# Kernel tuning notes

Hardware: AMD Instinct MI355X
Metric: run time of the kernel (lower is better)

The kernel has to match this reference:

```python
import jax, jax.numpy as jnp
import numpy as np

N_UNITS = 524288
BATCH = 16384


def setup_inputs() -> dict:
    key = jax.random.key(0)
    ks = jax.random.split(key, 10)
    left_feats = jax.random.normal(ks[0], (N_UNITS, 9), dtype=jnp.float32)
    right_feats = jax.random.normal(ks[1], (N_UNITS, 9), dtype=jnp.float32)
    left_seg = jnp.sort(jax.random.randint(ks[2], (N_UNITS,), 0, BATCH, dtype=jnp.int32))
    right_seg = jnp.sort(jax.random.randint(ks[3], (N_UNITS,), 0, BATCH, dtype=jnp.int32))
    W1 = jax.random.normal(ks[4], (9, 64), dtype=jnp.float32) * (1.0 / np.sqrt(9))
    b1 = jax.random.normal(ks[5], (64,), dtype=jnp.float32) * 0.01
    Wc1 = jax.random.normal(ks[6], (128, 32), dtype=jnp.float32) * (1.0 / np.sqrt(128))
    bc1 = jax.random.normal(ks[7], (32,), dtype=jnp.float32) * 0.01
    Wc2 = jax.random.normal(ks[8], (32, 1), dtype=jnp.float32) * (1.0 / np.sqrt(32))
    bc2 = jax.random.normal(ks[9], (1,), dtype=jnp.float32) * 0.01
    return {"left_feats": left_feats, "right_feats": right_feats,
            "left_seg": left_seg, "right_seg": right_seg,
            "W1": W1, "b1": b1, "Wc1": Wc1, "bc1": bc1, "Wc2": Wc2, "bc2": bc2}


def _pooled_features(feats, seg, W1, b1):
    # per-unit MLP 9 -> 64 with ReLU, then ragged sum-pool per instance
    h = jax.nn.relu(feats @ W1 + b1)                      # [N, 64]
    return jax.ops.segment_sum(h, seg, num_segments=BATCH)  # [B, 64]


def reference(left_feats, right_feats, left_seg, right_seg, W1, b1, Wc1, bc1, Wc2, bc2):
    left = _pooled_features(left_feats, left_seg, W1, b1)    # [B, 64]
    right = _pooled_features(right_feats, right_seg, W1, b1)  # [B, 64]
    combined = jnp.concatenate([left, right], axis=1)         # [B, 128]
    hidden = jax.nn.relu(combined @ Wc1 + bc1)                # [B, 32]
    logits = hidden @ Wc2 + bc2                               # [B, 1]
    return jax.nn.sigmoid(jnp.squeeze(logits, axis=-1))       # [B]
```

## Files before the change

### kernel.cpp

```cpp
#include <hip/hip_runtime.h>
#include <math.h>

#define BATCH_C 16384
#define SPW 2

typedef float f32x4  __attribute__((ext_vector_type(4)));
typedef f32x4 __attribute__((aligned(4))) f32x4_u;
typedef float f32x16 __attribute__((ext_vector_type(16)));
typedef short s16x8  __attribute__((ext_vector_type(8)));

typedef union { unsigned u[4]; s16x8 v; } abfrag_t;

static __device__ inline unsigned rlo_f(float x) {
    unsigned u = __float_as_uint(x);
    return (u + 0x7fffu + ((u >> 16) & 1u)) >> 16;
}
static __device__ inline unsigned rhi_f(float x) {
    unsigned u = __float_as_uint(x);
    return (u + 0x7fffu + ((u >> 16) & 1u)) & 0xffff0000u;
}

__global__ __launch_bounds__(256) void seg_starts_kernel(
    const int* __restrict__ lseg, const int* __restrict__ rseg, int n,
    int* __restrict__ lstart, int* __restrict__ rstart)
{
    const int* __restrict__ seg = blockIdx.y ? rseg : lseg;
    int* __restrict__ start = blockIdx.y ? rstart : lstart;
    int i = blockIdx.x * blockDim.x + threadIdx.x;
    if (i >= n) return;
    int s = seg[i];
    int prev = (i == 0) ? -1 : seg[i - 1];
    for (int b = prev + 1; b <= s; ++b) start[b] = i;
    if (i == n - 1) {
        for (int b = s + 1; b <= BATCH_C; ++b) start[b] = n;
    }
}

__global__ __launch_bounds__(256, 2) void fused_kernel(
    const float* __restrict__ lfeats, const float* __restrict__ rfeats,
    const int* __restrict__ lstart, const int* __restrict__ rstart,
    const float* __restrict__ W1, const float* __restrict__ b1,
    const float* __restrict__ Wc1, const float* __restrict__ bc1,
    const float* __restrict__ Wc2, const float* __restrict__ bc2,
    float* __restrict__ out, int nunits)
{
    const int lane = threadIdx.x & 63;
    const int wv   = threadIdx.x >> 6;
    const int S0   = (blockIdx.x * 4 + wv) * SPW;
    const int r    = lane & 31;
    const int hh   = lane >> 5;
    const int nmax = nunits - 1;
    const int ofs1 = hh ? 5 : 4;

    __shared__ __align__(16) short sBh[2][32][16];
    __shared__ __align__(16) short sBl[2][32][16];
    __shared__ __align__(16) float rowbuf[4][SPW][128];

    {
        const int t    = threadIdx.x;
        const int tile = t >> 7;
        const int col  = (t >> 2) & 31;
        const int k0   = (t & 3) * 4;
        const int ch   = tile * 32 + col;
#pragma unroll
        for (int q = 0; q < 4; ++q) {
            const int k = k0 + q;
            float v = 0.0f;
            if (k < 9) v = W1[k * 64 + ch];
            else if (k == 9) v = b1[ch];
            unsigned hi = rlo_f(v);
            float d = v - __uint_as_float(hi << 16);
            sBh[tile][col][k] = (short)hi;
            sBl[tile][col][k] = (short)rlo_f(d);
        }
    }
    __syncthreads();

    const s16x8 bh0 = *reinterpret_cast<const s16x8*>(&sBh[0][r][hh * 8]);
    const s16x8 bh1 = *reinterpret_cast<const s16x8*>(&sBh[1][r][hh * 8]);
    const s16x8 bl0 = *reinterpret_cast<const s16x8*>(&sBl[0][r][hh * 8]);
    const s16x8 bl1 = *reinterpret_cast<const s16x8*>(&sBl[1][r][hh * 8]);

    const f32x16 kZ = (f32x16)0.0f;

    rowbuf[wv][0][lane] = 0.0f;  rowbuf[wv][0][64 + lane] = 0.0f;
    rowbuf[wv][1][lane] = 0.0f;  rowbuf[wv][1][64 + lane] = 0.0f;

    const int bidx = S0 + (lane <= SPW ? lane : SPW);
    const int svl = lstart[bidx];
    const int svr = rstart[bidx];
    const int sLv = __shfl(svl, 0, 64);
    const int e1L = __shfl(svl, 1, 64);
    const int e2L = __shfl(svl, 2, 64);
    const int sRv = __shfl(svr, 0, 64);
    const int e1R = __shfl(svr, 1, 64);
    const int e2R = __shfl(svr, 2, 64);
    const int endL = e2L, endR = e2R;

#define FETCH_(F, POS, Q0,Q1,Q2,Q3,Q4,Q5,Q6,Q7) do {                      \
        int u_ = (POS) + r; if (u_ > nmax) u_ = nmax;                     \
        const float* fp_ = (F) + (size_t)u_ * 9;                          \
        f32x4 x0_ = *reinterpret_cast<const f32x4_u*>(fp_);               \
        f32x4 x1_ = *reinterpret_cast<const f32x4_u*>(fp_ + ofs1);        \
        Q0 = hh ? x1_.w : x0_.x;                                          \
        Q1 = x0_.y; Q2 = x0_.z; Q3 = x0_.w;                               \
        Q4 = x1_.x; Q5 = x1_.y; Q6 = x1_.z; Q7 = x1_.w;                   \
    } while (0)

#define CONV_(Q0,Q1,Q2,Q3,Q4,Q5,Q6,Q7, CNT, AH, AL) do {                  \
    unsigned u0_=__float_as_uint(Q0), u1_=__float_as_uint(Q1),            \
             u2_=__float_as_uint(Q2), u3_=__float_as_uint(Q3),            \
             u4_=__float_as_uint(Q4), u5_=__float_as_uint(Q5),            \
             u6_=__float_as_uint(Q6), u7_=__float_as_uint(Q7);            \
    float d0_=Q0-__uint_as_float(u0_&0xffff0000u);                        \
    float d1_=Q1-__uint_as_float(u1_&0xffff0000u);                        \
    float d2_=Q2-__uint_as_float(u2_&0xffff0000u);                        \
    float d3_=Q3-__uint_as_float(u3_&0xffff0000u);                        \
    float d4_=Q4-__uint_as_float(u4_&0xffff0000u);                        \
    float d5_=Q5-__uint_as_float(u5_&0xffff0000u);                        \
    float d6_=Q6-__uint_as_float(u6_&0xffff0000u);                        \
    float d7_=Q7-__uint_as_float(u7_&0xffff0000u);                        \
    unsigned h01_=(u0_>>16)|(hh?0x3F800000u:(u1_&0xffff0000u));           \
    unsigned l01_=rlo_f(d0_)|(hh?0u:rhi_f(d1_));                          \
    unsigned h23_=(u2_>>16)|(u3_&0xffff0000u);                            \
    unsigned h45_=(u4_>>16)|(u5_&0xffff0000u);                            \
    unsigned h67_=(u6_>>16)|(u7_&0xffff0000u);                            \
    unsigned l23_=rlo_f(d2_)|rhi_f(d3_);                                  \
    unsigned l45_=rlo_f(d4_)|rhi_f(d5_);                                  \
    unsigned l67_=rlo_f(d6_)|rhi_f(d7_);                                  \
    const bool v_ = (r < (CNT));                                          \
    const bool k_ = v_ && (hh == 0);                                      \
    AH.u[0]=v_?h01_:0u; AL.u[0]=v_?l01_:0u;                               \
    AH.u[1]=k_?h23_:0u; AL.u[1]=k_?l23_:0u;                               \
    AH.u[2]=k_?h45_:0u; AL.u[2]=k_?l45_:0u;                               \
    AH.u[3]=k_?h67_:0u; AL.u[3]=k_?l67_:0u;                               \
} while (0)

#define MFMAEPI_(AH, AL, A0, A1) do {                                     \
    f32x16 c0_ = __builtin_amdgcn_mfma_f32_32x32x16_bf16(AL.v, bh0, kZ, 0,0,0); \
    c0_ = __builtin_amdgcn_mfma_f32_32x32x16_bf16(AH.v, bl0, c0_, 0,0,0); \
    c0_ = __builtin_amdgcn_mfma_f32_32x32x16_bf16(AH.v, bh0, c0_, 0,0,0); \
    f32x16 c1_ = __builtin_amdgcn_mfma_f32_32x32x16_bf16(AL.v, bh1, kZ, 0,0,0); \
    c1_ = __builtin_amdgcn_mfma_f32_32x32x16_bf16(AH.v, bl1, c1_, 0,0,0); \
    c1_ = __builtin_amdgcn_mfma_f32_32x32x16_bf16(AH.v, bh1, c1_, 0,0,0); \
    float sA_=0.f,sB_=0.f,sC_=0.f,sD_=0.f,tA_=0.f,tB_=0.f,tC_=0.f,tD_=0.f;\
    _Pragma("unroll")                                                     \
    for (int t_=0; t_<4; ++t_) {                                          \
        sA_+=fmaxf(c0_[t_],0.f);    sB_+=fmaxf(c0_[t_+4],0.f);            \
        sC_+=fmaxf(c0_[t_+8],0.f);  sD_+=fmaxf(c0_[t_+12],0.f);           \
        tA_+=fmaxf(c1_[t_],0.f);    tB_+=fmaxf(c1_[t_+4],0.f);            \
        tC_+=fmaxf(c1_[t_+8],0.f);  tD_+=fmaxf(c1_[t_+12],0.f);           \
    }                                                                     \
    A0 += (sA_+sB_)+(sC_+sD_);                                            \
    A1 += (tA_+tB_)+(tC_+tD_);                                            \
} while (0)

#define STEP_(S) do {                                                     \
    int cnt_ = ec##S - base##S; if (cnt_ > 32) cnt_ = 32;                 \
    abfrag_t AH_, AL_;                                                    \
    CONV_(p0##S,p1##S,p2##S,p3##S,p4##S,p5##S,p6##S,p7##S, cnt_, AH_, AL_);\
    int nxt_ = base##S + cnt_;                                            \
    int fpos_ = (nxt_ < end##S) ? nxt_ : 0;  \
    FETCH_(f##S, fpos_, p0##S,p1##S,p2##S,p3##S,p4##S,p5##S,p6##S,p7##S); \
    MFMAEPI_(AH_, AL_, ac0##S, ac1##S);                                   \
    base##S = nxt_;                                                       \
} while (0)

#define FLUSH_(S, SIDEOFS) do {                                           \
    if (base##S >= ec##S) {                                               \
        ac0##S += __shfl_xor(ac0##S, 32, 64);                             \
        ac1##S += __shfl_xor(ac1##S, 32, 64);                             \
        if (cs##S < SPW)                                                  \
            rowbuf[wv][cs##S][(SIDEOFS) + lane] = hh ? ac1##S : ac0##S;   \
        ac0##S = 0.0f; ac1##S = 0.0f;                                     \
        ++cs##S; ec##S = e2##S;                                           \
    }                                                                     \
} while (0)

    const float* __restrict__ fL = lfeats;
    const float* __restrict__ fR = rfeats;
    int baseL = sLv, baseR = sRv;
    int csL, ecL, csR, ecR;
    if (baseL >= e1L) { csL = 1; ecL = e2L; } else { csL = 0; ecL = e1L; }
    if (baseR >= e1R) { csR = 1; ecR = e2R; } else { csR = 0; ecR = e1R; }
    float ac0L = 0.f, ac1L = 0.f, ac0R = 0.f, ac1R = 0.f;
    float p0L=0,p1L=0,p2L=0,p3L=0,p4L=0,p5L=0,p6L=0,p7L=0;
    float p0R=0,p1R=0,p2R=0,p3R=0,p4R=0,p5R=0,p6R=0,p7R=0;

    if (baseL < endL) FETCH_(fL, baseL, p0L,p1L,p2L,p3L,p4L,p5L,p6L,p7L);
    if (baseR < endR) FETCH_(fR, baseR, p0R,p1R,p2R,p3R,p4R,p5R,p6R,p7R);

    bool aL = baseL < endL, aR = baseR < endR;
    while (aL && aR) {
        STEP_(L);
        STEP_(R);
        FLUSH_(L, 0);
        FLUSH_(R, 64);
        aL = baseL < endL; aR = baseR < endR;
    }
    while (aL) { STEP_(L); FLUSH_(L, 0);  aL = baseL < endL; }
    while (aR) { STEP_(R); FLUSH_(R, 64); aR = baseR < endR; }

#undef FLUSH_
#undef STEP_
#undef MFMAEPI_
#undef CONV_
#undef FETCH_

    asm volatile("s_waitcnt lgkmcnt(0)" ::: "memory");

    {
        const int j = lane & 31;
        const float* __restrict__ rb = &rowbuf[wv][hh][0];
        const float* __restrict__ wc = Wc1 + j;

        float accA = bc1[j], accB = 0.0f;
#pragma unroll 8
        for (int k = 0; k < 128; k += 4) {
            f32x4 v = *reinterpret_cast<const f32x4*>(rb + k);
            accA = fmaf(v.x, wc[(k + 0) * 32], accA);
            accB = fmaf(v.y, wc[(k + 1) * 32], accB);
            accA = fmaf(v.z, wc[(k + 2) * 32], accA);
            accB = fmaf(v.w, wc[(k + 3) * 32], accB);
        }
        float hsv = fmaxf(accA + accB, 0.0f) * Wc2[j];
#pragma unroll
        for (int off = 16; off > 0; off >>= 1) hsv += __shfl_xor(hsv, off, 64);

        if (j == 0) {
            float logit = hsv + bc2[0];
            out[S0 + hh] = 1.0f / (1.0f + expf(-logit));
        }
    }
}

extern "C" void kernel_launch(void* const* d_in, const int* in_sizes, int n_in,
                              void* d_out, int out_size, void* d_ws, size_t ws_size,
                              hipStream_t stream)
{
    const float* lfeats = (const float*)d_in[0];
    const float* rfeats = (const float*)d_in[1];
    const int*   lseg   = (const int*)d_in[2];
    const int*   rseg   = (const int*)d_in[3];
    const float* W1     = (const float*)d_in[4];
    const float* b1     = (const float*)d_in[5];
    const float* Wc1    = (const float*)d_in[6];
    const float* bc1    = (const float*)d_in[7];
    const float* Wc2    = (const float*)d_in[8];
    const float* bc2    = (const float*)d_in[9];
    float* out = (float*)d_out;

    const int n = in_sizes[2];

    int* lstart = (int*)d_ws;
    int* rstart = lstart + (BATCH_C + 16);

    seg_starts_kernel<<<dim3((n + 255) / 256, 2), 256, 0, stream>>>(
        lseg, rseg, n, lstart, rstart);

    fused_kernel<<<BATCH_C / (SPW * 4), 256, 0, stream>>>(
        lfeats, rfeats, lstart, rstart, W1, b1, Wc1, bc1, Wc2, bc2, out, n);
}
```

Baseline: 37.33 us.

## Partition pooling by fixed unit windows with boundary partials and separate head kernel

```diff
diff --git a/kernel.cpp b/kernel.cpp
--- a/kernel.cpp
+++ b/kernel.cpp
@@ -2,66 +2,53 @@
 #include <math.h>
 
 #define BATCH_C 16384
-#define SPW 2
+#define UPW 128
 
 typedef float f32x4  __attribute__((ext_vector_type(4)));
 typedef f32x4 __attribute__((aligned(4))) f32x4_u;
 typedef float f32x16 __attribute__((ext_vector_type(16)));
 typedef short s16x8  __attribute__((ext_vector_type(8)));
-
 typedef union { unsigned u[4]; s16x8 v; } abfrag_t;
 
 static __device__ inline unsigned rlo_f(float x) {
     unsigned u = __float_as_uint(x);
     return (u + 0x7fffu + ((u >> 16) & 1u)) >> 16;
 }
-static __device__ inline unsigned rhi_f(float x) {
-    unsigned u = __float_as_uint(x);
-    return (u + 0x7fffu + ((u >> 16) & 1u)) & 0xffff0000u;
-}
-
-__global__ __launch_bounds__(256) void seg_starts_kernel(
-    const int* __restrict__ lseg, const int* __restrict__ rseg, int n,
-    int* __restrict__ lstart, int* __restrict__ rstart)
-{
-    const int* __restrict__ seg = blockIdx.y ? rseg : lseg;
-    int* __restrict__ start = blockIdx.y ? rstart : lstart;
-    int i = blockIdx.x * blockDim.x + threadIdx.x;
-    if (i >= n) return;
-    int s = seg[i];
-    int prev = (i == 0) ? -1 : seg[i - 1];
-    for (int b = prev + 1; b <= s; ++b) start[b] = i;
-    if (i == n - 1) {
-        for (int b = s + 1; b <= BATCH_C; ++b) start[b] = n;
-    }
-}
-
-__global__ __launch_bounds__(256, 2) void fused_kernel(
+
+__global__ __launch_bounds__(256, 4) void pool_dense(
     const float* __restrict__ lfeats, const float* __restrict__ rfeats,
-    const int* __restrict__ lstart, const int* __restrict__ rstart,
+    const int* __restrict__ lseg, const int* __restrict__ rseg,
+    int* __restrict__ lstart, int* __restrict__ rstart,
     const float* __restrict__ W1, const float* __restrict__ b1,
-    const float* __restrict__ Wc1, const float* __restrict__ bc1,
-    const float* __restrict__ Wc2, const float* __restrict__ bc2,
-    float* __restrict__ out, int nunits)
+    float* __restrict__ pooled,
+    float* __restrict__ pFl, float* __restrict__ pLl,
+    float* __restrict__ pFr, float* __restrict__ pLr,
+    int n)
 {
     const int lane = threadIdx.x & 63;
     const int wv   = threadIdx.x >> 6;
-    const int S0   = (blockIdx.x * 4 + wv) * SPW;
+    const int side = blockIdx.y;
+    const int wgid = blockIdx.x * 4 + wv;
+    const int lo   = wgid * UPW;
     const int r    = lane & 31;
     const int hh   = lane >> 5;
-    const int nmax = nunits - 1;
+    const int nmax = n - 1;
     const int ofs1 = hh ? 5 : 4;
+    const unsigned khi = hh ? 0u : 0xffffffffu;
+    const int sideofs = side * 64;
+
+    const float* __restrict__ feats = side ? rfeats : lfeats;
+    const int*   __restrict__ sg    = side ? rseg : lseg;
+    int* __restrict__ stw  = side ? rstart : lstart;
+    float* __restrict__ pFs = side ? pFr : pFl;
+    float* __restrict__ pLs = side ? pLr : pLl;
 
     __shared__ __align__(16) short sBh[2][32][16];
     __shared__ __align__(16) short sBl[2][32][16];
-    __shared__ __align__(16) float rowbuf[4][SPW][128];
-
     {
-        const int t    = threadIdx.x;
-        const int tile = t >> 7;
-        const int col  = (t >> 2) & 31;
-        const int k0   = (t & 3) * 4;
-        const int ch   = tile * 32 + col;
+        const int t = threadIdx.x;
+        const int tile = t >> 7, col = (t >> 2) & 31, k0 = (t & 3) * 4;
+        const int ch = tile * 32 + col;
 #pragma unroll
         for (int q = 0; q < 4; ++q) {
             const int k = k0 + q;
@@ -75,31 +62,33 @@
         }
     }
     __syncthreads();
-
     const s16x8 bh0 = *reinterpret_cast<const s16x8*>(&sBh[0][r][hh * 8]);
     const s16x8 bh1 = *reinterpret_cast<const s16x8*>(&sBh[1][r][hh * 8]);
     const s16x8 bl0 = *reinterpret_cast<const s16x8*>(&sBl[0][r][hh * 8]);
     const s16x8 bl1 = *reinterpret_cast<const s16x8*>(&sBl[1][r][hh * 8]);
-
     const f32x16 kZ = (f32x16)0.0f;
 
-    rowbuf[wv][0][lane] = 0.0f;  rowbuf[wv][0][64 + lane] = 0.0f;
-    rowbuf[wv][1][lane] = 0.0f;  rowbuf[wv][1][64 + lane] = 0.0f;
-
-    const int bidx = S0 + (lane <= SPW ? lane : SPW);
-    const int svl = lstart[bidx];
-    const int svr = rstart[bidx];
-    const int sLv = __shfl(svl, 0, 64);
-    const int e1L = __shfl(svl, 1, 64);
-    const int e2L = __shfl(svl, 2, 64);
-    const int sRv = __shfl(svr, 0, 64);
-    const int e1R = __shfl(svr, 1, 64);
-    const int e2R = __shfl(svr, 2, 64);
-    const int endL = e2L, endR = e2R;
-
-#define FETCH_(F, POS, Q0,Q1,Q2,Q3,Q4,Q5,Q6,Q7) do {                      \
-        int u_ = (POS) + r; if (u_ > nmax) u_ = nmax;                     \
-        const float* fp_ = (F) + (size_t)u_ * 9;                          \
+    const int u0 = lo + lane, u1 = lo + 64 + lane;
+    const int s0v = sg[u0 > nmax ? nmax : u0];
+    const int s1v = sg[u1 > nmax ? nmax : u1];
+    const int p0v = sg[u0 > 0 ? u0 - 1 : 0];
+    const int p1v = sg[(u1 - 1) > nmax ? nmax : (u1 - 1)];
+    {
+        int pe0 = (u0 == 0) ? -1 : p0v;
+        for (int b = pe0 + 1; b <= s0v; ++b) stw[b] = u0;
+        for (int b = p1v + 1; b <= s1v; ++b) stw[b] = u1;
+        if (u1 == nmax) for (int b = s1v + 1; b <= BATCH_C; ++b) stw[b] = n;
+    }
+    const bool bd0 = (lane != 0) && (s0v != p0v);
+    const bool bd1 = (s1v != p1v);
+    const unsigned long long mm0 = __ballot(bd0);
+    const unsigned long long mm1 = __ballot(bd1);
+    const unsigned wm0 = (unsigned)mm0, wm1 = (unsigned)(mm0 >> 32);
+    const unsigned wm2 = (unsigned)mm1, wm3 = (unsigned)(mm1 >> 32);
+
+#define FETCHD(POS, Q0,Q1,Q2,Q3,Q4,Q5,Q6,Q7) do {                         \
+        int uu_ = (POS) + r; if (uu_ > nmax) uu_ = nmax;                  \
+        const float* fp_ = feats + (size_t)uu_ * 9;                       \
         f32x4 x0_ = *reinterpret_cast<const f32x4_u*>(fp_);               \
         f32x4 x1_ = *reinterpret_cast<const f32x4_u*>(fp_ + ofs1);        \
         Q0 = hh ? x1_.w : x0_.x;                                          \
@@ -107,7 +96,7 @@
         Q4 = x1_.x; Q5 = x1_.y; Q6 = x1_.z; Q7 = x1_.w;                   \
     } while (0)
 
-#define CONV_(Q0,Q1,Q2,Q3,Q4,Q5,Q6,Q7, CNT, AH, AL) do {                  \
+#define CONVD(Q0,Q1,Q2,Q3,Q4,Q5,Q6,Q7, AH, AL) do {                       \
     unsigned u0_=__float_as_uint(Q0), u1_=__float_as_uint(Q1),            \
              u2_=__float_as_uint(Q2), u3_=__float_as_uint(Q3),            \
              u4_=__float_as_uint(Q4), u5_=__float_as_uint(Q5),            \
@@ -120,29 +109,27 @@
     float d5_=Q5-__uint_as_float(u5_&0xffff0000u);                        \
     float d6_=Q6-__uint_as_float(u6_&0xffff0000u);                        \
     float d7_=Q7-__uint_as_float(u7_&0xffff0000u);                        \
-    unsigned h01_=(u0_>>16)|(hh?0x3F800000u:(u1_&0xffff0000u));           \
-    unsigned l01_=rlo_f(d0_)|(hh?0u:rhi_f(d1_));                          \
-    unsigned h23_=(u2_>>16)|(u3_&0xffff0000u);                            \
-    unsigned h45_=(u4_>>16)|(u5_&0xffff0000u);                            \
-    unsigned h67_=(u6_>>16)|(u7_&0xffff0000u);                            \
-    unsigned l23_=rlo_f(d2_)|rhi_f(d3_);                                  \
-    unsigned l45_=rlo_f(d4_)|rhi_f(d5_);                                  \
-    unsigned l67_=rlo_f(d6_)|rhi_f(d7_);                                  \
-    const bool v_ = (r < (CNT));                                          \
-    const bool k_ = v_ && (hh == 0);                                      \
-    AH.u[0]=v_?h01_:0u; AL.u[0]=v_?l01_:0u;                               \
-    AH.u[1]=k_?h23_:0u; AL.u[1]=k_?l23_:0u;                               \
-    AH.u[2]=k_?h45_:0u; AL.u[2]=k_?l45_:0u;                               \
-    AH.u[3]=k_?h67_:0u; AL.u[3]=k_?l67_:0u;                               \
-} while (0)
-
-#define MFMAEPI_(AH, AL, A0, A1) do {                                     \
-    f32x16 c0_ = __builtin_amdgcn_mfma_f32_32x32x16_bf16(AL.v, bh0, kZ, 0,0,0); \
+    AH.u[0] = hh ? ((u0_>>16)|0x3F800000u) : ((u0_>>16)|(u1_&0xffff0000u));\
+    AL.u[0] = hh ? (__float_as_uint(d0_)>>16)                             \
+                 : ((__float_as_uint(d0_)>>16)|(__float_as_uint(d1_)&0xffff0000u));\
+    AH.u[1] = khi & ((u2_>>16)|(u3_&0xffff0000u));                        \
+    AL.u[1] = khi & ((__float_as_uint(d2_)>>16)|(__float_as_uint(d3_)&0xffff0000u));\
+    AH.u[2] = khi & ((u4_>>16)|(u5_&0xffff0000u));                        \
+    AL.u[2] = khi & ((__float_as_uint(d4_)>>16)|(__float_as_uint(d5_)&0xffff0000u));\
+    AH.u[3] = khi & ((u6_>>16)|(u7_&0xffff0000u));                        \
+    AL.u[3] = khi & ((__float_as_uint(d6_)>>16)|(__float_as_uint(d7_)&0xffff0000u));\
+} while (0)
+
+#define MFMAC(AH, AL) do {                                                \
+    c0_ = __builtin_amdgcn_mfma_f32_32x32x16_bf16(AL.v, bh0, kZ, 0,0,0);  \
     c0_ = __builtin_amdgcn_mfma_f32_32x32x16_bf16(AH.v, bl0, c0_, 0,0,0); \
     c0_ = __builtin_amdgcn_mfma_f32_32x32x16_bf16(AH.v, bh0, c0_, 0,0,0); \
-    f32x16 c1_ = __builtin_amdgcn_mfma_f32_32x32x16_bf16(AL.v, bh1, kZ, 0,0,0); \
+    c1_ = __builtin_amdgcn_mfma_f32_32x32x16_bf16(AL.v, bh1, kZ, 0,0,0);  \
     c1_ = __builtin_amdgcn_mfma_f32_32x32x16_bf16(AH.v, bl1, c1_, 0,0,0); \
     c1_ = __builtin_amdgcn_mfma_f32_32x32x16_bf16(AH.v, bh1, c1_, 0,0,0); \
+} while (0)
+
+#define FULLSUM do {                                                      \
     float sA_=0.f,sB_=0.f,sC_=0.f,sD_=0.f,tA_=0.f,tB_=0.f,tC_=0.f,tD_=0.f;\
     _Pragma("unroll")                                                     \
     for (int t_=0; t_<4; ++t_) {                                          \
@@ -151,62 +138,131 @@
         tA_+=fmaxf(c1_[t_],0.f);    tB_+=fmaxf(c1_[t_+4],0.f);            \
         tC_+=fmaxf(c1_[t_+8],0.f);  tD_+=fmaxf(c1_[t_+12],0.f);           \
     }                                                                     \
-    A0 += (sA_+sB_)+(sC_+sD_);                                            \
-    A1 += (tA_+tB_)+(tC_+tD_);                                            \
-} while (0)
-
-#define STEP_(S) do {                                                     \
-    int cnt_ = ec##S - base##S; if (cnt_ > 32) cnt_ = 32;                 \
+    acc0 += (sA_+sB_)+(sC_+sD_);                                          \
+    acc1 += (tA_+tB_)+(tC_+tD_);                                          \
+} while (0)
+
+#define RANGESUM(LOV, HIV) do {                                           \
+    _Pragma("unroll")                                                     \
+    for (int t_=0; t_<16; ++t_) {                                         \
+        const int rowt_ = (t_&3) + 8*(t_>>2) + 4*hh;                      \
+        const bool in_ = (rowt_ >= (LOV)) && (rowt_ < (HIV));             \
+        acc0 += in_ ? fmaxf(c0_[t_],0.f) : 0.f;                           \
+        acc1 += in_ ? fmaxf(c1_[t_],0.f) : 0.f;                           \
+    }                                                                     \
+} while (0)
+
+#define FLUSHSEG(BP, BN) do {                                             \
+    float fs0_ = acc0 + __shfl_xor(acc0, 32, 64);                         \
+    float fs1_ = acc1 + __shfl_xor(acc1, 32, 64);                         \
+    float ov_ = (lane >= 32) ? fs1_ : fs0_;                               \
+    if (nflush == 0) pFs[(size_t)wgid*64 + lane] = ov_;                   \
+    else pooled[(size_t)(BP)*128 + sideofs + lane] = ov_;                 \
+    ++nflush; acc0 = 0.f; acc1 = 0.f;                                     \
+    for (int e_=(BP)+1; e_<(BN); ++e_)                                    \
+        pooled[(size_t)e_*128 + sideofs + lane] = 0.0f;                   \
+} while (0)
+
+#define WINDOW(WK, MASKV, Q0,Q1,Q2,Q3,Q4,Q5,Q6,Q7, DOPF) do {             \
     abfrag_t AH_, AL_;                                                    \
-    CONV_(p0##S,p1##S,p2##S,p3##S,p4##S,p5##S,p6##S,p7##S, cnt_, AH_, AL_);\
-    int nxt_ = base##S + cnt_;                                            \
-    int fpos_ = (nxt_ < end##S) ? nxt_ : 0;  \
-    FETCH_(f##S, fpos_, p0##S,p1##S,p2##S,p3##S,p4##S,p5##S,p6##S,p7##S); \
-    MFMAEPI_(AH_, AL_, ac0##S, ac1##S);                                   \
-    base##S = nxt_;                                                       \
-} while (0)
-
-#define FLUSH_(S, SIDEOFS) do {                                           \
-    if (base##S >= ec##S) {                                               \
-        ac0##S += __shfl_xor(ac0##S, 32, 64);                             \
-        ac1##S += __shfl_xor(ac1##S, 32, 64);                             \
-        if (cs##S < SPW)                                                  \
-            rowbuf[wv][cs##S][(SIDEOFS) + lane] = hh ? ac1##S : ac0##S;   \
-        ac0##S = 0.0f; ac1##S = 0.0f;                                     \
-        ++cs##S; ec##S = e2##S;                                           \
+    CONVD(Q0,Q1,Q2,Q3,Q4,Q5,Q6,Q7, AH_, AL_);                             \
+    f32x16 c0_, c1_;                                                      \
+    MFMAC(AH_, AL_);                                                      \
+    if (DOPF) { FETCHD(lo + ((WK)+2)*32, Q0,Q1,Q2,Q3,Q4,Q5,Q6,Q7); }      \
+    unsigned bm_ = (MASKV);                                               \
+    if (bm_ == 0u) { FULLSUM; }                                           \
+    else {                                                                \
+        int prev_ = 0;                                                    \
+        while (bm_) {                                                     \
+            int p_ = __builtin_ctz(bm_); bm_ &= bm_ - 1u;                 \
+            RANGESUM(prev_, p_);                                          \
+            int gi_ = (WK)*32 + p_;                                       \
+            int bp_ = (gi_ - 1 < 64) ? __shfl(s0v, gi_ - 1, 64)           \
+                                     : __shfl(s1v, gi_ - 65, 64);         \
+            int bn_ = (gi_ < 64) ? __shfl(s0v, gi_, 64)                   \
+                                 : __shfl(s1v, gi_ - 64, 64);             \
+            bp_ = __builtin_amdgcn_readfirstlane(bp_);                    \
+            bn_ = __builtin_amdgcn_readfirstlane(bn_);                    \
+            FLUSHSEG(bp_, bn_);                                           \
+            prev_ = p_;                                                   \
+        }                                                                 \
+        RANGESUM(prev_, 32);                                              \
     }                                                                     \
 } while (0)
 
-    const float* __restrict__ fL = lfeats;
-    const float* __restrict__ fR = rfeats;
-    int baseL = sLv, baseR = sRv;
-    int csL, ecL, csR, ecR;
-    if (baseL >= e1L) { csL = 1; ecL = e2L; } else { csL = 0; ecL = e1L; }
-    if (baseR >= e1R) { csR = 1; ecR = e2R; } else { csR = 0; ecR = e1R; }
-    float ac0L = 0.f, ac1L = 0.f, ac0R = 0.f, ac1R = 0.f;
-    float p0L=0,p1L=0,p2L=0,p3L=0,p4L=0,p5L=0,p6L=0,p7L=0;
-    float p0R=0,p1R=0,p2R=0,p3R=0,p4R=0,p5R=0,p6R=0,p7R=0;
-
-    if (baseL < endL) FETCH_(fL, baseL, p0L,p1L,p2L,p3L,p4L,p5L,p6L,p7L);
-    if (baseR < endR) FETCH_(fR, baseR, p0R,p1R,p2R,p3R,p4R,p5R,p6R,p7R);
-
-    bool aL = baseL < endL, aR = baseR < endR;
-    while (aL && aR) {
-        STEP_(L);
-        STEP_(R);
-        FLUSH_(L, 0);
-        FLUSH_(R, 64);
-        aL = baseL < endL; aR = baseR < endR;
-    }
-    while (aL) { STEP_(L); FLUSH_(L, 0);  aL = baseL < endL; }
-    while (aR) { STEP_(R); FLUSH_(R, 64); aR = baseR < endR; }
-
-#undef FLUSH_
-#undef STEP_
-#undef MFMAEPI_
-#undef CONV_
-#undef FETCH_
-
+    float a0,a1,a2,a3,a4,a5,a6,a7;
+    float b0v,b1v,b2v,b3v,b4v,b5v,b6v,b7v;
+    FETCHD(lo,      a0,a1,a2,a3,a4,a5,a6,a7);
+    FETCHD(lo + 32, b0v,b1v,b2v,b3v,b4v,b5v,b6v,b7v);
+
+    float acc0 = 0.f, acc1 = 0.f;
+    int nflush = 0;
+
+    WINDOW(0, wm0, a0,a1,a2,a3,a4,a5,a6,a7, 1);
+    WINDOW(1, wm1, b0v,b1v,b2v,b3v,b4v,b5v,b6v,b7v, 1);
+    WINDOW(2, wm2, a0,a1,a2,a3,a4,a5,a6,a7, 0);
+    WINDOW(3, wm3, b0v,b1v,b2v,b3v,b4v,b5v,b6v,b7v, 0);
+
+    {
+        float fm0 = acc0 + __shfl_xor(acc0, 32, 64);
+        float fm1 = acc1 + __shfl_xor(acc1, 32, 64);
+        float fov = (lane >= 32) ? fm1 : fm0;
+        pLs[(size_t)wgid*64 + lane] = fov;
+        if (nflush == 0) pFs[(size_t)wgid*64 + lane] = fov;
+    }
+#undef WINDOW
+#undef FLUSHSEG
+#undef RANGESUM
+#undef FULLSUM
+#undef MFMAC
+#undef CONVD
+#undef FETCHD
+}
+
+__global__ __launch_bounds__(256) void head2_kernel(
+    const int* __restrict__ lstart, const int* __restrict__ rstart,
+    const int* __restrict__ lseg, const int* __restrict__ rseg,
+    const float* __restrict__ pooled,
+    const float* __restrict__ pFl, const float* __restrict__ pLl,
+    const float* __restrict__ pFr, const float* __restrict__ pLr,
+    const float* __restrict__ Wc1, const float* __restrict__ bc1,
+    const float* __restrict__ Wc2, const float* __restrict__ bc2,
+    float* __restrict__ out)
+{
+    const int lane = threadIdx.x & 63;
+    const int wv   = threadIdx.x >> 6;
+    const int hh   = lane >> 5;
+    const int S0   = (blockIdx.x * 4 + wv) * 2;
+
+    __shared__ __align__(16) float rowbuf[4][2][128];
+
+    for (int rowi = 0; rowi < 2; ++rowi) {
+        const int b = S0 + rowi;
+#pragma unroll
+        for (int sd = 0; sd < 2; ++sd) {
+            const int* st = sd ? rstart : lstart;
+            const int* sgp = sd ? rseg : lseg;
+            const float* pFp = sd ? pFr : pFl;
+            const float* pLp = sd ? pLr : pLl;
+            const int sb = st[b];
+            const int se = st[b + 1];
+            const int wa = sb >> 7;
+            const bool owned = ((sb & 127) == 0) || (se > (wa << 7) + 127);
+            float v;
+            if (owned) {
+                v = 0.0f;
+                const int wb = (se > sb) ? ((se - 1) >> 7) : (wa - 1);
+                for (int w = wa; w <= wb; ++w) {
+                    const int key = sgp[w << 7];
+                    const float* src = (key == b) ? pFp : pLp;
+                    v += src[(size_t)w * 64 + lane];
+                }
+            } else {
+                v = pooled[(size_t)b * 128 + sd * 64 + lane];
+            }
+            rowbuf[wv][rowi][sd * 64 + lane] = v;
+        }
+    }
     asm volatile("s_waitcnt lgkmcnt(0)" ::: "memory");
 
     {
@@ -250,14 +306,22 @@
     const float* bc2    = (const float*)d_in[9];
     float* out = (float*)d_out;
 
-    const int n = in_sizes[2];
-
-    int* lstart = (int*)d_ws;
+    const int n  = in_sizes[2];
+    const int nw = n / UPW;
+
+    float* pooled = (float*)d_ws;
+    float* pFl = pooled + (size_t)BATCH_C * 128;
+    float* pLl = pFl + (size_t)nw * 64;
+    float* pFr = pLl + (size_t)nw * 64;
+    float* pLr = pFr + (size_t)nw * 64;
+    int* lstart = (int*)(pLr + (size_t)nw * 64);
     int* rstart = lstart + (BATCH_C + 16);
 
-    seg_starts_kernel<<<dim3((n + 255) / 256, 2), 256, 0, stream>>>(
-        lseg, rseg, n, lstart, rstart);
-
-    fused_kernel<<<BATCH_C / (SPW * 4), 256, 0, stream>>>(
-        lfeats, rfeats, lstart, rstart, W1, b1, Wc1, bc1, Wc2, bc2, out, n);
+    pool_dense<<<dim3(nw / 4, 2), 256, 0, stream>>>(
+        lfeats, rfeats, lseg, rseg, lstart, rstart, W1, b1,
+        pooled, pFl, pLl, pFr, pLr, n);
+
+    head2_kernel<<<BATCH_C / 8, 256, 0, stream>>>(
+        lstart, rstart, lseg, rseg, pooled, pFl, pLl, pFr, pLr,
+        Wc1, bc1, Wc2, bc2, out);
 }
```

Measured after the change: 40.97 us. +9.8%, slower.
